# Optimization experiments

Hardware: AMD Instinct MI355X
Metric: run time of the kernel (lower is better)

Reference implementation:

```python
import jax, jax.numpy as jnp
import numpy as np

B, N, DIM = 4, 1024, 768
H, GP = 12, 64
HD = DIM // H
SCALE = HD ** -0.5


def setup_inputs() -> dict:
    key = jax.random.key(0)
    ks = jax.random.split(key, 7)
    s = DIM ** -0.5
    return {
        "x": jax.random.normal(ks[0], (B, N, DIM), dtype=jnp.float32),
        "W_qkv": jax.random.normal(ks[1], (3 * DIM, DIM), dtype=jnp.float32) * s,
        "b_qkv": jnp.zeros((3 * DIM,), dtype=jnp.float32),
        "W_gp": jax.random.normal(ks[2], (GP, DIM), dtype=jnp.float32) * s,
        "alpha": jax.random.normal(ks[3], (1, H, 1, 1), dtype=jnp.float32),
        "W_proj": jax.random.normal(ks[4], (DIM, DIM), dtype=jnp.float32) * s,
        "b_proj": jnp.zeros((DIM,), dtype=jnp.float32),
    }


def reference(x, W_qkv, b_qkv, W_gp, alpha, W_proj, b_proj):
    b, n, c = x.shape
    # qkv projection, split into heads: [b, h, n, hd]
    qkv = x @ W_qkv.T + b_qkv
    q, k, v = jnp.split(qkv, 3, axis=-1)
    def to_heads(t):
        return t.reshape(b, n, H, HD).transpose(0, 2, 1, 3)
    q, k, v = to_heads(q), to_heads(k), to_heads(v)

    # raw attention scores [b, h, n, n]
    attn = jnp.einsum('bhnd,bhmd->bhnm', q, k) * SCALE

    # group similarity: gp weight viewed as [h, gp, hd]
    gp = W_gp.reshape(H, GP, HD)
    gw = jnp.einsum('bhnd,hmd->bhnm', v, gp)          # [b, h, n, gp]
    gw = jax.nn.gelu(gw, approximate=False)           # exact GELU (torch default)
    gw = jax.nn.softmax(gw, axis=-1)
    G = jnp.einsum('bhnm,bhkm->bhnk', gw, gw)         # [b, h, n, n]

    # gated combination
    attn = jax.nn.softmax(attn * G, axis=-1)
    a = jax.nn.sigmoid(alpha)                          # [1, h, 1, 1]
    A = (1.0 - a) * attn + a * G
    # column-sum renormalization (sum over query dim 2)
    A = A / (A.sum(axis=2, keepdims=True) + 1e-8)

    out = jnp.einsum('bhnm,bhmd->bhnd', A, v)
    out = out.transpose(0, 2, 1, 3).reshape(b, n, c)
    return out @ W_proj.T + b_proj
```

## Files before the change

### kernel.cpp

```cpp
#include <hip/hip_runtime.h>
#include <math.h>

namespace {

constexpr int kN   = 1024;
constexpr int kDim = 768;
constexpr int kH   = 12;
constexpr int kBH  = 48;
constexpr float kScale = 0.125f;

typedef __attribute__((ext_vector_type(8))) short short8;
typedef __attribute__((ext_vector_type(4))) short short4v;
typedef __attribute__((ext_vector_type(4))) float f32x4;
typedef __attribute__((ext_vector_type(16))) float f32x16;
typedef __attribute__((ext_vector_type(4))) uint uint4v;

#define MFMA(a, b, c)   __builtin_amdgcn_mfma_f32_16x16x32_bf16(a, b, c, 0, 0, 0)
#define MFMA32(a, b, c) __builtin_amdgcn_mfma_f32_32x32x16_bf16(a, b, c, 0, 0, 0)

__device__ __forceinline__ ushort f2bf(float f) {
  uint u = __builtin_bit_cast(uint, f);
  u += 0x7fffu + ((u >> 16) & 1u);
  return (ushort)(u >> 16);
}
__device__ __forceinline__ float bf2f(ushort h) {
  uint u = ((uint)h) << 16;
  return __builtin_bit_cast(float, u);
}
__device__ __forceinline__ void split8(const float* f, short8& hi, short8& lo) {
  #pragma unroll
  for (int i = 0; i < 8; i++) {
    const ushort h = f2bf(f[i]);
    hi[i] = (short)h;
    lo[i] = (short)f2bf(f[i] - bf2f(h));
  }
}
__device__ __forceinline__ uint packbf(float a, float b) {
  return (uint)f2bf(a) | ((uint)f2bf(b) << 16);
}

__device__ __forceinline__ void gl16(const short* g, short* l) {
  __builtin_amdgcn_global_load_lds(
      (const __attribute__((address_space(1))) void*)g,
      (__attribute__((address_space(3))) void*)l, 16, 0, 0);
}

__device__ __forceinline__ short8 frag(const short* t, int row, int chunk) {
  return *(const short8*)(t + row * 64 + ((chunk ^ (row & 7)) << 3));
}

template<int ROWS, int W>
__device__ __forceinline__ void stage_tile(short* dst, const short* src,
                                           int stride, int w, int l) {
  #pragma unroll
  for (int c = 0; c < ROWS / 8; c += W) {
    const int cc = c + w;
    const int row0 = cc << 3;
    const int row = row0 + (l >> 3);
    const int ch = (l & 7) ^ (row & 7);
    gl16(src + (size_t)row * stride + (ch << 3), dst + row0 * 64);
  }
}

__global__ __launch_bounds__(256) void k_split(const float* __restrict__ src,
                                               short* __restrict__ h,
                                               short* __restrict__ l) {
  const size_t i = ((size_t)blockIdx.x * 256 + threadIdx.x) * 4;
  const float4 f = *(const float4*)(src + i);
  const float ff[4] = {f.x, f.y, f.z, f.w};
  short4v hv, lv;
  #pragma unroll
  for (int j = 0; j < 4; j++) {
    const ushort u = f2bf(ff[j]);
    hv[j] = (short)u;
    lv[j] = (short)f2bf(ff[j] - bf2f(u));
  }
  *(short4v*)(h + i) = hv;
  *(short4v*)(l + i) = lv;
}

__global__ __launch_bounds__(512) void k_qkv(const short* __restrict__ xh,
                                             const short* __restrict__ xl,
                                             const short* __restrict__ wh,
                                             const short* __restrict__ wl,
                                             const float* __restrict__ bias,
                                             short* __restrict__ qh, short* __restrict__ ql,
                                             short* __restrict__ kh, short* __restrict__ kl,
                                             short* __restrict__ vh, short* __restrict__ vl) {
  __shared__ __align__(16) short sb[2][32768];
  const int bx = blockIdx.x, by = blockIdx.y;
  const int tid = threadIdx.x, w = tid >> 6, lane = tid & 63;
  const int wr = w >> 2, wc = w & 3;
  const short* Asrc_h = xh + (size_t)(by * 128) * kDim;
  const short* Asrc_l = xl + (size_t)(by * 128) * kDim;
  const short* Bsrc_h = wh + (size_t)(bx * 128) * kDim;
  const short* Bsrc_l = wl + (size_t)(bx * 128) * kDim;

  f32x4 acc[4][2] = {};
  {
    short* nb = sb[0];
    stage_tile<128, 8>(nb,          Asrc_h, kDim, w, lane);
    stage_tile<128, 8>(nb + 8192,   Asrc_l, kDim, w, lane);
    stage_tile<128, 8>(nb + 16384,  Bsrc_h, kDim, w, lane);
    stage_tile<128, 8>(nb + 24576,  Bsrc_l, kDim, w, lane);
  }
  int p = 0;
  #pragma unroll 1
  for (int t = 0; t < 12; ++t) {
    __syncthreads();
    if (t < 11) {
      const int k0 = (t + 1) * 64;
      short* nb = sb[p ^ 1];
      stage_tile<128, 8>(nb,         Asrc_h + k0, kDim, w, lane);
      stage_tile<128, 8>(nb + 8192,  Asrc_l + k0, kDim, w, lane);
      stage_tile<128, 8>(nb + 16384, Bsrc_h + k0, kDim, w, lane);
      stage_tile<128, 8>(nb + 24576, Bsrc_l + k0, kDim, w, lane);
    }
    const short* cb = sb[p];
    #pragma unroll
    for (int s = 0; s < 2; ++s) {
      const int ch = (s << 2) + (lane >> 4);
      short8 af[4], alf[4], bf_[2], blf[2];
      #pragma unroll
      for (int i = 0; i < 4; i++) {
        const int ar = wr * 64 + i * 16 + (lane & 15);
        af[i]  = frag(cb, ar, ch);
        alf[i] = frag(cb + 8192, ar, ch);
      }
      #pragma unroll
      for (int j = 0; j < 2; j++) {
        const int br = wc * 32 + j * 16 + (lane & 15);
        bf_[j] = frag(cb + 16384, br, ch);
        blf[j] = frag(cb + 24576, br, ch);
      }
      #pragma unroll
      for (int i = 0; i < 4; i++)
        #pragma unroll
        for (int j = 0; j < 2; j++) {
          acc[i][j] = MFMA(af[i], bf_[j], acc[i][j]);
          acc[i][j] = MFMA(af[i], blf[j], acc[i][j]);
          acc[i][j] = MFMA(alf[i], bf_[j], acc[i][j]);
        }
    }
    p ^= 1;
  }
  #pragma unroll
  for (int j = 0; j < 2; j++) {
    const int col = bx * 128 + wc * 32 + j * 16 + (lane & 15);
    const int part = col / 768;
    const int rem = col - part * 768;
    const int hh = rem >> 6, d = rem & 63;
    short* dh = (part == 0) ? qh : ((part == 1) ? kh : vh);
    short* dl = (part == 0) ? ql : ((part == 1) ? kl : vl);
    const float bv = bias[col];
    const float scl = (part == 0) ? kScale : 1.0f;
    #pragma unroll
    for (int i = 0; i < 4; i++) {
      #pragma unroll
      for (int r = 0; r < 4; r++) {
        const int gr = by * 128 + wr * 64 + i * 16 + ((lane >> 4) << 2) + r;
        const int b = gr >> 10, n = gr & 1023;
        const float val = (acc[i][j][r] + bv) * scl;
        const ushort hu = f2bf(val);
        const size_t idx = (size_t)((b * kH + hh) * kN + n) * 64 + d;
        dh[idx] = (short)hu;
        dl[idx] = (short)f2bf(val - bf2f(hu));
      }
    }
  }
}

__global__ __launch_bounds__(512) void k_gw(const short* __restrict__ vh,
                                            const short* __restrict__ vl,
                                            const float* __restrict__ Wgp,
                                            short* __restrict__ gwh,
                                            short* __restrict__ gwl) {
  const int bh = blockIdx.x;
  const int h = bh % kH;
  const int n0 = blockIdx.y << 7;
  const int tid = threadIdx.x, w = tid >> 6, lane = tid & 63;
  __shared__ __align__(16) short gph[4096], gpl[4096];
  {
    const int r = tid >> 3, c = tid & 7;
    float f[8] __attribute__((aligned(16)));
    *(float4*)(f + 0) = *(const float4*)(Wgp + h * 4096 + r * 64 + c * 8);
    *(float4*)(f + 4) = *(const float4*)(Wgp + h * 4096 + r * 64 + c * 8 + 4);
    short8 hh, ll;
    split8(f, hh, ll);
    const int slot = c ^ (r & 7);
    *(short8*)(gph + r * 64 + slot * 8) = hh;
    *(short8*)(gpl + r * 64 + slot * 8) = ll;
  }
  short8 vhf[2], vlf[2];
  const size_t arow = (size_t)(bh * kN + n0 + w * 16 + (lane & 15)) * 64 + ((lane >> 4) << 3);
  vhf[0] = *(const short8*)(vh + arow); vhf[1] = *(const short8*)(vh + arow + 32);
  vlf[0] = *(const short8*)(vl + arow); vlf[1] = *(const short8*)(vl + arow + 32);
  __syncthreads();

  f32x4 aU[4] = {};
  #pragma unroll
  for (int msub = 0; msub < 4; msub++) {
    #pragma unroll
    for (int s = 0; s < 2; s++) {
      const int row = (msub << 4) + (lane & 15);
      const int ch = (s << 2) + (lane >> 4);
      const short8 bh_ = frag(gph, row, ch);
      const short8 bl_ = frag(gpl, row, ch);
      aU[msub] = MFMA(vhf[s], bh_, aU[msub]);
      aU[msub] = MFMA(vhf[s], bl_, aU[msub]);
      aU[msub] = MFMA(vlf[s], bh_, aU[msub]);
    }
  }
  #pragma unroll
  for (int r = 0; r < 4; r++) {
    float u[4];
    #pragma unroll
    for (int m = 0; m < 4; m++) {
      const float a = aU[m][r];
      u[m] = 0.5f * a * (1.0f + erff(a * 0.70710678118654752f));
    }
    float mx = fmaxf(fmaxf(u[0], u[1]), fmaxf(u[2], u[3]));
    #pragma unroll
    for (int msk = 1; msk < 16; msk <<= 1) mx = fmaxf(mx, __shfl_xor(mx, msk));
    float e[4], ssum = 0.f;
    #pragma unroll
    for (int m = 0; m < 4; m++) { e[m] = __expf(u[m] - mx); ssum += e[m]; }
    #pragma unroll
    for (int msk = 1; msk < 16; msk <<= 1) ssum += __shfl_xor(ssum, msk);
    const float inv = 1.0f / ssum;
    const int n = n0 + w * 16 + ((lane >> 4) << 2) + r;
    #pragma unroll
    for (int m = 0; m < 4; m++) {
      const float g = e[m] * inv;
      const ushort hu = f2bf(g);
      const size_t idx = (size_t)(bh * kN + n) * 64 + (m << 4) + (lane & 15);
      gwh[idx] = (short)hu;
      gwl[idx] = (short)f2bf(g - bf2f(hu));
    }
  }
}

__global__ __launch_bounds__(256) void k_vt(const short* __restrict__ vh,
                                            const float* __restrict__ rcolv,
                                            short* __restrict__ vtg) {
  const int bh = blockIdx.x;
  const int n0 = blockIdx.y << 6;
  __shared__ short t[64][80];
  const int tid = threadIdx.x;
  {
    const int n = tid >> 2, d0 = (tid & 3) << 4;
    const float rc = rcolv[bh * kN + n0 + n];
    const short8 a = *(const short8*)(vh + (size_t)(bh * kN + n0 + n) * 64 + d0);
    const short8 b = *(const short8*)(vh + (size_t)(bh * kN + n0 + n) * 64 + d0 + 8);
    #pragma unroll
    for (int i = 0; i < 8; ++i) {
      t[d0 + i][n]     = (short)f2bf(bf2f((ushort)a[i]) * rc);
      t[d0 + 8 + i][n] = (short)f2bf(bf2f((ushort)b[i]) * rc);
    }
  }
  __syncthreads();
  const int d = tid >> 2, j0 = (tid & 3) << 4;
  short* dst = vtg + (size_t)bh * 65536 + (size_t)d * 1024 + n0 + j0;
  *(short8*)(dst)     = *(const short8*)(&t[d][j0]);
  *(short8*)(dst + 8) = *(const short8*)(&t[d][j0 + 8]);
}

__global__ __launch_bounds__(256, 3) void k_denom(const short* __restrict__ qh,
                                                  const short* __restrict__ ql,
                                                  const short* __restrict__ kh,
                                                  const short* __restrict__ kl,
                                                  const short* __restrict__ gwh,
                                                  const short* __restrict__ gwl,
                                                  float* __restrict__ rdenom) {
  const int bh = blockIdx.x;
  const int n0 = blockIdx.y << 6;
  const int tid = threadIdx.x, w = tid >> 6, lane = tid & 63;
  const int lc = lane & 31, hl = lane >> 5;
  const int nw = w & 1, mh = w >> 1;
  __shared__ __align__(16) short sb[32768];
  __shared__ float part[4][32];
  const short* my = sb + mh * 16384;

  short8 qB[4], qlB[4], gB[4], glB[4];
  {
    const size_t nrow = (size_t)(bh * kN + n0 + nw * 32 + lc) * 64;
    #pragma unroll
    for (int ks = 0; ks < 4; ks++) {
      const int off = ks * 16 + (hl << 3);
      qB[ks]  = *(const short8*)(qh  + nrow + off);
      qlB[ks] = *(const short8*)(ql  + nrow + off);
      gB[ks]  = *(const short8*)(gwh + nrow + off);
      glB[ks] = *(const short8*)(gwl + nrow + off);
    }
  }
  float dsum = 0.f;
  #pragma unroll 1
  for (int t = 0; t < 8; ++t) {
    __syncthreads();
    const size_t mo0 = (size_t)(bh * kN + t * 64) * 64;
    const size_t mo1 = (size_t)(bh * kN + 512 + t * 64) * 64;
    stage_tile<64, 4>(sb,          kh  + mo0, 64, w, lane);
    stage_tile<64, 4>(sb + 4096,   kl  + mo0, 64, w, lane);
    stage_tile<64, 4>(sb + 8192,   gwh + mo0, 64, w, lane);
    stage_tile<64, 4>(sb + 12288,  gwl + mo0, 64, w, lane);
    stage_tile<64, 4>(sb + 16384,  kh  + mo1, 64, w, lane);
    stage_tile<64, 4>(sb + 20480,  kl  + mo1, 64, w, lane);
    stage_tile<64, 4>(sb + 24576,  gwh + mo1, 64, w, lane);
    stage_tile<64, 4>(sb + 28672,  gwl + mo1, 64, w, lane);
    __syncthreads();
    #pragma unroll
    for (int at = 0; at < 2; ++at) {
      f32x16 aS = {}, aG = {};
      #pragma unroll
      for (int ks = 0; ks < 4; ++ks) {
        const int row = at * 32 + lc;
        const int ck = ks * 2 + hl;
        const short8 Ah_ = frag(my, row, ck);
        const short8 Al_ = frag(my + 4096, row, ck);
        const short8 Eh_ = frag(my + 8192, row, ck);
        const short8 El_ = frag(my + 12288, row, ck);
        aS = MFMA32(Ah_, qB[ks], aS);
        aS = MFMA32(Al_, qB[ks], aS);
        aS = MFMA32(Ah_, qlB[ks], aS);
        aG = MFMA32(Eh_, gB[ks], aG);
        aG = MFMA32(El_, gB[ks], aG);
        aG = MFMA32(Eh_, glB[ks], aG);
      }
      #pragma unroll
      for (int r = 0; r < 16; ++r)
        dsum += __expf(aS[r] * aG[r]);
    }
  }
  dsum += __shfl_xor(dsum, 32);
  if (hl == 0) part[w][lc] = dsum;
  __syncthreads();
  if (tid < 64)
    rdenom[bh * kN + n0 + tid] =
        1.0f / (part[tid >> 5][tid & 31] + part[2 + (tid >> 5)][tid & 31]);
}

__global__ __launch_bounds__(256, 3) void k_colsum(const short* __restrict__ qh,
                                                   const short* __restrict__ ql,
                                                   const short* __restrict__ kh,
                                                   const short* __restrict__ kl,
                                                   const short* __restrict__ gwh,
                                                   const short* __restrict__ gwl,
                                                   const float* __restrict__ rdenom,
                                                   const float* __restrict__ alpha,
                                                   float* __restrict__ rcolv) {
  const int bh = blockIdx.x;
  const int m0 = blockIdx.y << 6;
  const int tid = threadIdx.x, w = tid >> 6, lane = tid & 63;
  const int lc = lane & 31, hl = lane >> 5;
  const int mw = w & 1, nh = w >> 1;
  __shared__ __align__(16) short sb[32768];
  __shared__ float part[4][32];
  __shared__ float rdl[2][64];
  const short* my = sb + nh * 16384;
  const float ah_ = 1.0f / (1.0f + __expf(-alpha[bh % kH]));
  const float om = 1.0f - ah_;

  short8 kB[4], klB[4], gB[4], glB[4];
  {
    const size_t mrow = (size_t)(bh * kN + m0 + mw * 32 + lc) * 64;
    #pragma unroll
    for (int ks = 0; ks < 4; ks++) {
      const int off = ks * 16 + (hl << 3);
      kB[ks]  = *(const short8*)(kh  + mrow + off);
      klB[ks] = *(const short8*)(kl  + mrow + off);
      gB[ks]  = *(const short8*)(gwh + mrow + off);
      glB[ks] = *(const short8*)(gwl + mrow + off);
    }
  }
  float csum = 0.f;
  #pragma unroll 1
  for (int t = 0; t < 8; ++t) {
    __syncthreads();
    const size_t no0 = (size_t)(bh * kN + t * 64) * 64;
    const size_t no1 = (size_t)(bh * kN + 512 + t * 64) * 64;
    stage_tile<64, 4>(sb,          qh  + no0, 64, w, lane);
    stage_tile<64, 4>(sb + 4096,   ql  + no0, 64, w, lane);
    stage_tile<64, 4>(sb + 8192,   gwh + no0, 64, w, lane);
    stage_tile<64, 4>(sb + 12288,  gwl + no0, 64, w, lane);
    stage_tile<64, 4>(sb + 16384,  qh  + no1, 64, w, lane);
    stage_tile<64, 4>(sb + 20480,  ql  + no1, 64, w, lane);
    stage_tile<64, 4>(sb + 24576,  gwh + no1, 64, w, lane);
    stage_tile<64, 4>(sb + 28672,  gwl + no1, 64, w, lane);
    if (tid < 128)
      rdl[tid >> 6][tid & 63] =
          rdenom[bh * kN + (tid >> 6) * 512 + t * 64 + (tid & 63)];
    __syncthreads();
    #pragma unroll
    for (int at = 0; at < 2; ++at) {
      f32x16 aS = {}, aG = {};
      #pragma unroll
      for (int ks = 0; ks < 4; ++ks) {
        const int row = at * 32 + lc;
        const int ck = ks * 2 + hl;
        const short8 Ah_ = frag(my, row, ck);
        const short8 Al_ = frag(my + 4096, row, ck);
        const short8 Eh_ = frag(my + 8192, row, ck);
        const short8 El_ = frag(my + 12288, row, ck);
        aS = MFMA32(Ah_, kB[ks], aS);
        aS = MFMA32(Al_, kB[ks], aS);
        aS = MFMA32(Ah_, klB[ks], aS);
        aG = MFMA32(Eh_, gB[ks], aG);
        aG = MFMA32(El_, gB[ks], aG);
        aG = MFMA32(Eh_, glB[ks], aG);
      }
      #pragma unroll
      for (int r = 0; r < 16; ++r) {
        const int nr = at * 32 + (r & 3) + ((r >> 2) << 3) + (hl << 2);
        const float g = aG[r];
        csum += om * (__expf(aS[r] * g) * rdl[nh][nr]) + ah_ * g;
      }
    }
  }
  csum += __shfl_xor(csum, 32);
  if (hl == 0) part[w][lc] = csum;
  __syncthreads();
  if (tid < 64)
    rcolv[bh * kN + m0 + tid] =
        1.0f / (part[tid >> 5][tid & 31] + part[2 + (tid >> 5)][tid & 31] + 1e-8f);
}

__global__ __launch_bounds__(512, 2) void k_out(const short* __restrict__ qh,
                                                const short* __restrict__ ql,
                                                const short* __restrict__ kh,
                                                const short* __restrict__ kl,
                                                const short* __restrict__ vtg,
                                                const short* __restrict__ gwh,
                                                const short* __restrict__ gwl,
                                                const float* __restrict__ rdenom,
                                                const float* __restrict__ alpha,
                                                short* __restrict__ ctxh,
                                                short* __restrict__ ctxl) {
  const int bh = blockIdx.x;
  const int h = bh % kH;
  const int b = bh / kH;
  const int n0 = blockIdx.y << 7;
  const int tid = threadIdx.x, w = tid >> 6, lane = tid & 63;
  const int lc = lane & 31, hl = lane >> 5;
  const int nw = w & 3, mh = w >> 2;
  __shared__ __align__(16) short sb[40960];
  const float ah_ = 1.0f / (1.0f + __expf(-alpha[h]));
  const float om = 1.0f - ah_;
  const short* my = sb + mh * 20480;

  short8 qB[4], qlB[4], gB[4], glB[4];
  {
    const size_t nrow = (size_t)(bh * kN + n0 + nw * 32 + lc) * 64;
    #pragma unroll
    for (int ks = 0; ks < 4; ks++) {
      const int off = ks * 16 + (hl << 3);
      qB[ks]  = *(const short8*)(qh  + nrow + off);
      qlB[ks] = *(const short8*)(ql  + nrow + off);
      gB[ks]  = *(const short8*)(gwh + nrow + off);
      glB[ks] = *(const short8*)(gwl + nrow + off);
    }
  }
  const float rdn = rdenom[bh * kN + n0 + nw * 32 + lc];
  f32x16 oac[2] = {};

  #pragma unroll 1
  for (int t = 0; t < 8; ++t) {
    __syncthreads();
    const size_t mo0 = (size_t)(bh * kN + t * 64) * 64;
    const size_t mo1 = (size_t)(bh * kN + 512 + t * 64) * 64;
    stage_tile<64, 8>(sb,          kh  + mo0, 64, w, lane);
    stage_tile<64, 8>(sb + 4096,   kl  + mo0, 64, w, lane);
    stage_tile<64, 8>(sb + 8192,   gwh + mo0, 64, w, lane);
    stage_tile<64, 8>(sb + 12288,  gwl + mo0, 64, w, lane);
    stage_tile<64, 8>(sb + 16384,  vtg + (size_t)bh * 65536 + t * 64, kN, w, lane);
    stage_tile<64, 8>(sb + 20480,  kh  + mo1, 64, w, lane);
    stage_tile<64, 8>(sb + 24576,  kl  + mo1, 64, w, lane);
    stage_tile<64, 8>(sb + 28672,  gwh + mo1, 64, w, lane);
    stage_tile<64, 8>(sb + 32768,  gwl + mo1, 64, w, lane);
    stage_tile<64, 8>(sb + 36864,  vtg + (size_t)bh * 65536 + 512 + t * 64, kN, w, lane);
    __syncthreads();
    short8 pf[4];
    #pragma unroll
    for (int at = 0; at < 2; ++at) {
      f32x16 aS = {}, aG = {};
      #pragma unroll
      for (int ks = 0; ks < 4; ++ks) {
        const int row = at * 32 + lc;
        const int ck = ks * 2 + hl;
        const short8 Ah_ = frag(my, row, ck);
        const short8 Al_ = frag(my + 4096, row, ck);
        const short8 Eh_ = frag(my + 8192, row, ck);
        const short8 El_ = frag(my + 12288, row, ck);
        aS = MFMA32(Ah_, qB[ks], aS);
        aS = MFMA32(Al_, qB[ks], aS);
        aS = MFMA32(Ah_, qlB[ks], aS);
        aG = MFMA32(Eh_, gB[ks], aG);
        aG = MFMA32(El_, gB[ks], aG);
        aG = MFMA32(Eh_, glB[ks], aG);
      }
      float a[16];
      #pragma unroll
      for (int r = 0; r < 16; ++r) {
        const float g = aG[r];
        const float p = __expf(aS[r] * g) * rdn;
        a[r] = om * p + ah_ * g;
      }
      uint W[8], Ws[8];
      #pragma unroll
      for (int j = 0; j < 8; ++j) W[j] = packbf(a[2 * j], a[2 * j + 1]);
      #pragma unroll
      for (int j = 0; j < 8; ++j) Ws[j] = __shfl_xor(W[j], 32);
      {
        uint4v b0, b1;
        b0[0] = hl ? Ws[2] : W[0];  b0[1] = hl ? Ws[3] : W[1];
        b0[2] = hl ? W[2]  : Ws[0]; b0[3] = hl ? W[3]  : Ws[1];
        b1[0] = hl ? Ws[6] : W[4];  b1[1] = hl ? Ws[7] : W[5];
        b1[2] = hl ? W[6]  : Ws[4]; b1[3] = hl ? W[7]  : Ws[5];
        pf[at * 2 + 0] = __builtin_bit_cast(short8, b0);
        pf[at * 2 + 1] = __builtin_bit_cast(short8, b1);
      }
    }
    #pragma unroll
    for (int dt = 0; dt < 2; ++dt)
      #pragma unroll
      for (int ks = 0; ks < 4; ++ks) {
        const short8 va = frag(my + 16384, dt * 32 + lc, ks * 2 + hl);
        oac[dt] = MFMA32(va, pf[ks], oac[dt]);
      }
  }
  __syncthreads();
  float* buf = (float*)sb;
  if (mh == 1) {
    #pragma unroll
    for (int dt = 0; dt < 2; ++dt)
      #pragma unroll
      for (int r = 0; r < 16; ++r) {
        const int d = dt * 32 + (r & 3) + ((r >> 2) << 3) + (hl << 2);
        buf[(nw * 32 + lc) * 68 + d] = oac[dt][r];
      }
  }
  __syncthreads();
  if (mh == 0) {
    #pragma unroll
    for (int dt = 0; dt < 2; ++dt)
      #pragma unroll
      for (int r = 0; r < 16; ++r) {
        const int d = dt * 32 + (r & 3) + ((r >> 2) << 3) + (hl << 2);
        const int idx = (nw * 32 + lc) * 68 + d;
        buf[idx] = oac[dt][r] + buf[idx];
      }
  }
  __syncthreads();
  {
    const int rowi = tid >> 2;
    const int d0 = (tid & 3) << 4;
    float f[16] __attribute__((aligned(16)));
    #pragma unroll
    for (int j = 0; j < 4; ++j)
      *(float4*)(f + 4 * j) = *(const float4*)(&buf[rowi * 68 + d0 + 4 * j]);
    const int n = n0 + rowi;
    short* dsth = ctxh + (size_t)(b * kN + n) * kDim + h * 64 + d0;
    short* dstl = ctxl + (size_t)(b * kN + n) * kDim + h * 64 + d0;
    #pragma unroll
    for (int g8 = 0; g8 < 2; ++g8) {
      short8 hi, lo;
      split8(f + 8 * g8, hi, lo);
      *(short8*)(dsth + 8 * g8) = hi;
      *(short8*)(dstl + 8 * g8) = lo;
    }
  }
}

__global__ __launch_bounds__(512) void k_proj(const short* __restrict__ ch_,
                                              const short* __restrict__ cl_,
                                              const short* __restrict__ wh,
                                              const short* __restrict__ wl,
                                              const float* __restrict__ bias,
                                              float* __restrict__ out) {
  __shared__ __align__(16) short sb[2][32768];
  const int bx = blockIdx.x, by = blockIdx.y;
  const int tid = threadIdx.x, w = tid >> 6, lane = tid & 63;
  const int wr = w >> 2, wc = w & 3;
  const short* Asrc_h = ch_ + (size_t)(by * 128) * kDim;
  const short* Asrc_l = cl_ + (size_t)(by * 128) * kDim;
  const short* Bsrc_h = wh + (size_t)(bx * 128) * kDim;
  const short* Bsrc_l = wl + (size_t)(bx * 128) * kDim;

  f32x4 acc[4][2] = {};
  {
    short* nb = sb[0];
    stage_tile<128, 8>(nb,         Asrc_h, kDim, w, lane);
    stage_tile<128, 8>(nb + 8192,  Asrc_l, kDim, w, lane);
    stage_tile<128, 8>(nb + 16384, Bsrc_h, kDim, w, lane);
    stage_tile<128, 8>(nb + 24576, Bsrc_l, kDim, w, lane);
  }
  int p = 0;
  #pragma unroll 1
  for (int t = 0; t < 12; ++t) {
    __syncthreads();
    if (t < 11) {
      const int k0 = (t + 1) * 64;
      short* nb = sb[p ^ 1];
      stage_tile<128, 8>(nb,         Asrc_h + k0, kDim, w, lane);
      stage_tile<128, 8>(nb + 8192,  Asrc_l + k0, kDim, w, lane);
      stage_tile<128, 8>(nb + 16384, Bsrc_h + k0, kDim, w, lane);
      stage_tile<128, 8>(nb + 24576, Bsrc_l + k0, kDim, w, lane);
    }
    const short* cb = sb[p];
    #pragma unroll
    for (int s = 0; s < 2; ++s) {
      const int ch = (s << 2) + (lane >> 4);
      short8 af[4], alf[4], bf_[2], blf[2];
      #pragma unroll
      for (int i = 0; i < 4; i++) {
        const int ar = wr * 64 + i * 16 + (lane & 15);
        af[i]  = frag(cb, ar, ch);
        alf[i] = frag(cb + 8192, ar, ch);
      }
      #pragma unroll
      for (int j = 0; j < 2; j++) {
        const int br = wc * 32 + j * 16 + (lane & 15);
        bf_[j] = frag(cb + 16384, br, ch);
        blf[j] = frag(cb + 24576, br, ch);
      }
      #pragma unroll
      for (int i = 0; i < 4; i++)
        #pragma unroll
        for (int j = 0; j < 2; j++) {
          acc[i][j] = MFMA(af[i], bf_[j], acc[i][j]);
          acc[i][j] = MFMA(af[i], blf[j], acc[i][j]);
          acc[i][j] = MFMA(alf[i], bf_[j], acc[i][j]);
          acc[i][j] = MFMA(alf[i], blf[j], acc[i][j]);
        }
    }
    p ^= 1;
  }
  #pragma unroll
  for (int j = 0; j < 2; j++) {
    const int col = bx * 128 + wc * 32 + j * 16 + (lane & 15);
    const float bv = bias[col];
    #pragma unroll
    for (int i = 0; i < 4; i++) {
      #pragma unroll
      for (int r = 0; r < 4; r++) {
        const int row = by * 128 + wr * 64 + i * 16 + ((lane >> 4) << 2) + r;
        out[(size_t)row * kDim + col] = acc[i][j][r] + bv;
      }
    }
  }
}

}

extern "C" void kernel_launch(void* const* d_in, const int* in_sizes, int n_in,
                              void* d_out, int out_size, void* d_ws, size_t ws_size,
                              hipStream_t stream) {
  const float* x     = (const float*)d_in[0];
  const float* Wqkv  = (const float*)d_in[1];
  const float* bqkv  = (const float*)d_in[2];
  const float* Wgp   = (const float*)d_in[3];
  const float* alpha = (const float*)d_in[4];
  const float* Wproj = (const float*)d_in[5];
  const float* bproj = (const float*)d_in[6];
  float* out = (float*)d_out;

  const size_t he = 3145728;
  short* qh  = (short*)d_ws;
  short* ql  = qh + he;
  short* kh  = ql + he;
  short* kl  = kh + he;
  short* vh  = kl + he;
  short* vl  = vh + he;
  short* gwh = vl + he;
  short* gwl = gwh + he;
  short* xh  = gwl + he;
  short* xl  = xh + he;
  float* rdenom = (float*)(xl + he);
  float* rcolv  = rdenom + (size_t)kBH * kN;

  short* Wqh = gwh;  short* Wql = gwl;
  short* vtg = vl;
  short* ctxh = xh;  short* ctxl = xl;
  short* Wph = qh;   short* Wpl = ql;

  k_split<<<3072, 256, 0, stream>>>(x, xh, xl);
  k_split<<<1728, 256, 0, stream>>>(Wqkv, Wqh, Wql);
  k_qkv  <<<dim3(18, 32), 512, 0, stream>>>(xh, xl, Wqh, Wql, bqkv,
                                            qh, ql, kh, kl, vh, vl);
  k_gw   <<<dim3(kBH, 8), 512, 0, stream>>>(vh, vl, Wgp, gwh, gwl);
  k_denom<<<dim3(kBH, 16), 256, 0, stream>>>(qh, ql, kh, kl, gwh, gwl, rdenom);
  k_colsum<<<dim3(kBH, 16), 256, 0, stream>>>(qh, ql, kh, kl, gwh, gwl,
                                              rdenom, alpha, rcolv);
  k_vt   <<<dim3(kBH, 16), 256, 0, stream>>>(vh, rcolv, vtg);
  k_out  <<<dim3(kBH, 8), 512, 0, stream>>>(qh, ql, kh, kl, vtg, gwh, gwl,
                                            rdenom, alpha, ctxh, ctxl);
  k_split<<<576, 256, 0, stream>>>(Wproj, Wph, Wpl);
  k_proj <<<dim3(6, 32), 512, 0, stream>>>(ctxh, ctxl, Wph, Wpl, bproj, out);
}
```

Before: 277.8 us.

## Halve key-tile size in attention kernels to shrink LDS and raise occupancy

The denom, colsum and output kernels now stage 32-row key tiles, one per half of the split key range, over 16 iterations instead of 64-row tiles over 8. This halves shared memory per block so more blocks fit per CU. k_out also drops from 512-thread, 128-query blocks to 256-thread, 64-query blocks with twice as many blocks, and loads the V^T tile with a swizzled direct global-to-LDS copy. The cost is twice as many barriers and staging rounds per block, and K/gw tiles are now reloaded by twice as many k_out blocks.

```diff
diff --git a/kernel.cpp b/kernel.cpp
--- a/kernel.cpp
+++ b/kernel.cpp
@@ -277,9 +277,8 @@
   const int tid = threadIdx.x, w = tid >> 6, lane = tid & 63;
   const int lc = lane & 31, hl = lane >> 5;
   const int nw = w & 1, mh = w >> 1;
-  __shared__ __align__(16) short sb[32768];
+  __shared__ __align__(16) short sb[16384];
   __shared__ float part[4][32];
-  const short* my = sb + mh * 16384;
 
   short8 qB[4], qlB[4], gB[4], glB[4];
   {
@@ -295,41 +294,38 @@
   }
   float dsum = 0.f;
   #pragma unroll 1
-  for (int t = 0; t < 8; ++t) {
-    __syncthreads();
-    const size_t mo0 = (size_t)(bh * kN + t * 64) * 64;
-    const size_t mo1 = (size_t)(bh * kN + 512 + t * 64) * 64;
-    stage_tile<64, 4>(sb,          kh  + mo0, 64, w, lane);
-    stage_tile<64, 4>(sb + 4096,   kl  + mo0, 64, w, lane);
-    stage_tile<64, 4>(sb + 8192,   gwh + mo0, 64, w, lane);
-    stage_tile<64, 4>(sb + 12288,  gwl + mo0, 64, w, lane);
-    stage_tile<64, 4>(sb + 16384,  kh  + mo1, 64, w, lane);
-    stage_tile<64, 4>(sb + 20480,  kl  + mo1, 64, w, lane);
-    stage_tile<64, 4>(sb + 24576,  gwh + mo1, 64, w, lane);
-    stage_tile<64, 4>(sb + 28672,  gwl + mo1, 64, w, lane);
-    __syncthreads();
-    #pragma unroll
-    for (int at = 0; at < 2; ++at) {
-      f32x16 aS = {}, aG = {};
-      #pragma unroll
-      for (int ks = 0; ks < 4; ++ks) {
-        const int row = at * 32 + lc;
-        const int ck = ks * 2 + hl;
-        const short8 Ah_ = frag(my, row, ck);
-        const short8 Al_ = frag(my + 4096, row, ck);
-        const short8 Eh_ = frag(my + 8192, row, ck);
-        const short8 El_ = frag(my + 12288, row, ck);
-        aS = MFMA32(Ah_, qB[ks], aS);
-        aS = MFMA32(Al_, qB[ks], aS);
-        aS = MFMA32(Ah_, qlB[ks], aS);
-        aG = MFMA32(Eh_, gB[ks], aG);
-        aG = MFMA32(El_, gB[ks], aG);
-        aG = MFMA32(Eh_, glB[ks], aG);
-      }
-      #pragma unroll
-      for (int r = 0; r < 16; ++r)
-        dsum += __expf(aS[r] * aG[r]);
-    }
+  for (int t = 0; t < 16; ++t) {
+    __syncthreads();
+    const size_t mo0 = (size_t)(bh * kN + t * 32) * 64;
+    const size_t mo1 = (size_t)(bh * kN + 512 + t * 32) * 64;
+    stage_tile<32, 4>(sb,                kh  + mo0, 64, w, lane);
+    stage_tile<32, 4>(sb + 2048,         kh  + mo1, 64, w, lane);
+    stage_tile<32, 4>(sb + 4096,         kl  + mo0, 64, w, lane);
+    stage_tile<32, 4>(sb + 4096 + 2048,  kl  + mo1, 64, w, lane);
+    stage_tile<32, 4>(sb + 8192,         gwh + mo0, 64, w, lane);
+    stage_tile<32, 4>(sb + 8192 + 2048,  gwh + mo1, 64, w, lane);
+    stage_tile<32, 4>(sb + 12288,        gwl + mo0, 64, w, lane);
+    stage_tile<32, 4>(sb + 12288 + 2048, gwl + mo1, 64, w, lane);
+    __syncthreads();
+    f32x16 aS = {}, aG = {};
+    #pragma unroll
+    for (int ks = 0; ks < 4; ++ks) {
+      const int row = mh * 32 + lc;
+      const int ck = ks * 2 + hl;
+      const short8 Ah_ = frag(sb, row, ck);
+      const short8 Al_ = frag(sb + 4096, row, ck);
+      const short8 Eh_ = frag(sb + 8192, row, ck);
+      const short8 El_ = frag(sb + 12288, row, ck);
+      aS = MFMA32(Ah_, qB[ks], aS);
+      aS = MFMA32(Al_, qB[ks], aS);
+      aS = MFMA32(Ah_, qlB[ks], aS);
+      aG = MFMA32(Eh_, gB[ks], aG);
+      aG = MFMA32(El_, gB[ks], aG);
+      aG = MFMA32(Eh_, glB[ks], aG);
+    }
+    #pragma unroll
+    for (int r = 0; r < 16; ++r)
+      dsum += __expf(aS[r] * aG[r]);
   }
   dsum += __shfl_xor(dsum, 32);
   if (hl == 0) part[w][lc] = dsum;
@@ -353,10 +349,9 @@
   const int tid = threadIdx.x, w = tid >> 6, lane = tid & 63;
   const int lc = lane & 31, hl = lane >> 5;
   const int mw = w & 1, nh = w >> 1;
-  __shared__ __align__(16) short sb[32768];
+  __shared__ __align__(16) short sb[16384];
   __shared__ float part[4][32];
-  __shared__ float rdl[2][64];
-  const short* my = sb + nh * 16384;
+  __shared__ float rdl[2][32];
   const float ah_ = 1.0f / (1.0f + __expf(-alpha[bh % kH]));
   const float om = 1.0f - ah_;
 
@@ -374,46 +369,43 @@
   }
   float csum = 0.f;
   #pragma unroll 1
-  for (int t = 0; t < 8; ++t) {
-    __syncthreads();
-    const size_t no0 = (size_t)(bh * kN + t * 64) * 64;
-    const size_t no1 = (size_t)(bh * kN + 512 + t * 64) * 64;
-    stage_tile<64, 4>(sb,          qh  + no0, 64, w, lane);
-    stage_tile<64, 4>(sb + 4096,   ql  + no0, 64, w, lane);
-    stage_tile<64, 4>(sb + 8192,   gwh + no0, 64, w, lane);
-    stage_tile<64, 4>(sb + 12288,  gwl + no0, 64, w, lane);
-    stage_tile<64, 4>(sb + 16384,  qh  + no1, 64, w, lane);
-    stage_tile<64, 4>(sb + 20480,  ql  + no1, 64, w, lane);
-    stage_tile<64, 4>(sb + 24576,  gwh + no1, 64, w, lane);
-    stage_tile<64, 4>(sb + 28672,  gwl + no1, 64, w, lane);
-    if (tid < 128)
-      rdl[tid >> 6][tid & 63] =
-          rdenom[bh * kN + (tid >> 6) * 512 + t * 64 + (tid & 63)];
-    __syncthreads();
-    #pragma unroll
-    for (int at = 0; at < 2; ++at) {
-      f32x16 aS = {}, aG = {};
-      #pragma unroll
-      for (int ks = 0; ks < 4; ++ks) {
-        const int row = at * 32 + lc;
-        const int ck = ks * 2 + hl;
-        const short8 Ah_ = frag(my, row, ck);
-        const short8 Al_ = frag(my + 4096, row, ck);
-        const short8 Eh_ = frag(my + 8192, row, ck);
-        const short8 El_ = frag(my + 12288, row, ck);
-        aS = MFMA32(Ah_, kB[ks], aS);
-        aS = MFMA32(Al_, kB[ks], aS);
-        aS = MFMA32(Ah_, klB[ks], aS);
-        aG = MFMA32(Eh_, gB[ks], aG);
-        aG = MFMA32(El_, gB[ks], aG);
-        aG = MFMA32(Eh_, glB[ks], aG);
-      }
-      #pragma unroll
-      for (int r = 0; r < 16; ++r) {
-        const int nr = at * 32 + (r & 3) + ((r >> 2) << 3) + (hl << 2);
-        const float g = aG[r];
-        csum += om * (__expf(aS[r] * g) * rdl[nh][nr]) + ah_ * g;
-      }
+  for (int t = 0; t < 16; ++t) {
+    __syncthreads();
+    const size_t no0 = (size_t)(bh * kN + t * 32) * 64;
+    const size_t no1 = (size_t)(bh * kN + 512 + t * 32) * 64;
+    stage_tile<32, 4>(sb,                qh  + no0, 64, w, lane);
+    stage_tile<32, 4>(sb + 2048,         qh  + no1, 64, w, lane);
+    stage_tile<32, 4>(sb + 4096,         ql  + no0, 64, w, lane);
+    stage_tile<32, 4>(sb + 4096 + 2048,  ql  + no1, 64, w, lane);
+    stage_tile<32, 4>(sb + 8192,         gwh + no0, 64, w, lane);
+    stage_tile<32, 4>(sb + 8192 + 2048,  gwh + no1, 64, w, lane);
+    stage_tile<32, 4>(sb + 12288,        gwl + no0, 64, w, lane);
+    stage_tile<32, 4>(sb + 12288 + 2048, gwl + no1, 64, w, lane);
+    if (tid < 64)
+      rdl[tid >> 5][tid & 31] =
+          rdenom[bh * kN + (tid >> 5) * 512 + t * 32 + (tid & 31)];
+    __syncthreads();
+    f32x16 aS = {}, aG = {};
+    #pragma unroll
+    for (int ks = 0; ks < 4; ++ks) {
+      const int row = nh * 32 + lc;
+      const int ck = ks * 2 + hl;
+      const short8 Ah_ = frag(sb, row, ck);
+      const short8 Al_ = frag(sb + 4096, row, ck);
+      const short8 Eh_ = frag(sb + 8192, row, ck);
+      const short8 El_ = frag(sb + 12288, row, ck);
+      aS = MFMA32(Ah_, kB[ks], aS);
+      aS = MFMA32(Al_, kB[ks], aS);
+      aS = MFMA32(Ah_, klB[ks], aS);
+      aG = MFMA32(Eh_, gB[ks], aG);
+      aG = MFMA32(El_, gB[ks], aG);
+      aG = MFMA32(Eh_, glB[ks], aG);
+    }
+    #pragma unroll
+    for (int r = 0; r < 16; ++r) {
+      const int nr = (r & 3) + ((r >> 2) << 3) + (hl << 2);
+      const float g = aG[r];
+      csum += om * (__expf(aS[r] * g) * rdl[nh][nr]) + ah_ * g;
     }
   }
   csum += __shfl_xor(csum, 32);
@@ -424,7 +416,7 @@
         1.0f / (part[tid >> 5][tid & 31] + part[2 + (tid >> 5)][tid & 31] + 1e-8f);
 }
 
-__global__ __launch_bounds__(512, 2) void k_out(const short* __restrict__ qh,
+__global__ __launch_bounds__(256, 3) void k_out(const short* __restrict__ qh,
                                                 const short* __restrict__ ql,
                                                 const short* __restrict__ kh,
                                                 const short* __restrict__ kl,
@@ -438,14 +430,13 @@
   const int bh = blockIdx.x;
   const int h = bh % kH;
   const int b = bh / kH;
-  const int n0 = blockIdx.y << 7;
+  const int n0 = blockIdx.y << 6;
   const int tid = threadIdx.x, w = tid >> 6, lane = tid & 63;
   const int lc = lane & 31, hl = lane >> 5;
-  const int nw = w & 3, mh = w >> 2;
-  __shared__ __align__(16) short sb[40960];
+  const int nw = w & 1, mh = w >> 1;
+  __shared__ __align__(16) short sb[20480];
   const float ah_ = 1.0f / (1.0f + __expf(-alpha[h]));
   const float om = 1.0f - ah_;
-  const short* my = sb + mh * 20480;
 
   short8 qB[4], qlB[4], gB[4], glB[4];
   {
@@ -460,70 +451,75 @@
     }
   }
   const float rdn = rdenom[bh * kN + n0 + nw * 32 + lc];
+  const short* vbh = vtg + (size_t)bh * 65536;
   f32x16 oac[2] = {};
 
   #pragma unroll 1
-  for (int t = 0; t < 8; ++t) {
-    __syncthreads();
-    const size_t mo0 = (size_t)(bh * kN + t * 64) * 64;
-    const size_t mo1 = (size_t)(bh * kN + 512 + t * 64) * 64;
-    stage_tile<64, 8>(sb,          kh  + mo0, 64, w, lane);
-    stage_tile<64, 8>(sb + 4096,   kl  + mo0, 64, w, lane);
-    stage_tile<64, 8>(sb + 8192,   gwh + mo0, 64, w, lane);
-    stage_tile<64, 8>(sb + 12288,  gwl + mo0, 64, w, lane);
-    stage_tile<64, 8>(sb + 16384,  vtg + (size_t)bh * 65536 + t * 64, kN, w, lane);
-    stage_tile<64, 8>(sb + 20480,  kh  + mo1, 64, w, lane);
-    stage_tile<64, 8>(sb + 24576,  kl  + mo1, 64, w, lane);
-    stage_tile<64, 8>(sb + 28672,  gwh + mo1, 64, w, lane);
-    stage_tile<64, 8>(sb + 32768,  gwl + mo1, 64, w, lane);
-    stage_tile<64, 8>(sb + 36864,  vtg + (size_t)bh * 65536 + 512 + t * 64, kN, w, lane);
-    __syncthreads();
-    short8 pf[4];
-    #pragma unroll
-    for (int at = 0; at < 2; ++at) {
-      f32x16 aS = {}, aG = {};
-      #pragma unroll
-      for (int ks = 0; ks < 4; ++ks) {
-        const int row = at * 32 + lc;
-        const int ck = ks * 2 + hl;
-        const short8 Ah_ = frag(my, row, ck);
-        const short8 Al_ = frag(my + 4096, row, ck);
-        const short8 Eh_ = frag(my + 8192, row, ck);
-        const short8 El_ = frag(my + 12288, row, ck);
-        aS = MFMA32(Ah_, qB[ks], aS);
-        aS = MFMA32(Al_, qB[ks], aS);
-        aS = MFMA32(Ah_, qlB[ks], aS);
-        aG = MFMA32(Eh_, gB[ks], aG);
-        aG = MFMA32(El_, gB[ks], aG);
-        aG = MFMA32(Eh_, glB[ks], aG);
-      }
-      float a[16];
-      #pragma unroll
-      for (int r = 0; r < 16; ++r) {
-        const float g = aG[r];
-        const float p = __expf(aS[r] * g) * rdn;
-        a[r] = om * p + ah_ * g;
-      }
+  for (int t = 0; t < 16; ++t) {
+    __syncthreads();
+    const size_t mo0 = (size_t)(bh * kN + t * 32) * 64;
+    const size_t mo1 = (size_t)(bh * kN + 512 + t * 32) * 64;
+    stage_tile<32, 4>(sb,                kh  + mo0, 64, w, lane);
+    stage_tile<32, 4>(sb + 2048,         kh  + mo1, 64, w, lane);
+    stage_tile<32, 4>(sb + 4096,         kl  + mo0, 64, w, lane);
+    stage_tile<32, 4>(sb + 4096 + 2048,  kl  + mo1, 64, w, lane);
+    stage_tile<32, 4>(sb + 8192,         gwh + mo0, 64, w, lane);
+    stage_tile<32, 4>(sb + 8192 + 2048,  gwh + mo1, 64, w, lane);
+    stage_tile<32, 4>(sb + 12288,        gwl + mo0, 64, w, lane);
+    stage_tile<32, 4>(sb + 12288 + 2048, gwl + mo1, 64, w, lane);
+    #pragma unroll
+    for (int c = 0; c < 8; c += 4) {
+      const int cc = c + w;
+      const int row0 = cc << 3;
+      const int row = row0 + (lane >> 3);
+      const int ch = (lane & 7) ^ (row & 7);
+      const int mg = ((ch >> 2) ? 512 : 0) + t * 32 + ((ch & 3) << 3);
+      gl16(vbh + (size_t)row * 1024 + mg, sb + 16384 + row0 * 64);
+    }
+    __syncthreads();
+    f32x16 aS = {}, aG = {};
+    #pragma unroll
+    for (int ks = 0; ks < 4; ++ks) {
+      const int row = mh * 32 + lc;
+      const int ck = ks * 2 + hl;
+      const short8 Ah_ = frag(sb, row, ck);
+      const short8 Al_ = frag(sb + 4096, row, ck);
+      const short8 Eh_ = frag(sb + 8192, row, ck);
+      const short8 El_ = frag(sb + 12288, row, ck);
+      aS = MFMA32(Ah_, qB[ks], aS);
+      aS = MFMA32(Al_, qB[ks], aS);
+      aS = MFMA32(Ah_, qlB[ks], aS);
+      aG = MFMA32(Eh_, gB[ks], aG);
+      aG = MFMA32(El_, gB[ks], aG);
+      aG = MFMA32(Eh_, glB[ks], aG);
+    }
+    float a[16];
+    #pragma unroll
+    for (int r = 0; r < 16; ++r) {
+      const float g = aG[r];
+      const float p = __expf(aS[r] * g) * rdn;
+      a[r] = om * p + ah_ * g;
+    }
+    short8 pf[2];
+    {
       uint W[8], Ws[8];
       #pragma unroll
       for (int j = 0; j < 8; ++j) W[j] = packbf(a[2 * j], a[2 * j + 1]);
       #pragma unroll
       for (int j = 0; j < 8; ++j) Ws[j] = __shfl_xor(W[j], 32);
-      {
-        uint4v b0, b1;
-        b0[0] = hl ? Ws[2] : W[0];  b0[1] = hl ? Ws[3] : W[1];
-        b0[2] = hl ? W[2]  : Ws[0]; b0[3] = hl ? W[3]  : Ws[1];
-        b1[0] = hl ? Ws[6] : W[4];  b1[1] = hl ? Ws[7] : W[5];
-        b1[2] = hl ? W[6]  : Ws[4]; b1[3] = hl ? W[7]  : Ws[5];
-        pf[at * 2 + 0] = __builtin_bit_cast(short8, b0);
-        pf[at * 2 + 1] = __builtin_bit_cast(short8, b1);
-      }
+      uint4v b0, b1;
+      b0[0] = hl ? Ws[2] : W[0];  b0[1] = hl ? Ws[3] : W[1];
+      b0[2] = hl ? W[2]  : Ws[0]; b0[3] = hl ? W[3]  : Ws[1];
+      b1[0] = hl ? Ws[6] : W[4];  b1[1] = hl ? Ws[7] : W[5];
+      b1[2] = hl ? W[6]  : Ws[4]; b1[3] = hl ? W[7]  : Ws[5];
+      pf[0] = __builtin_bit_cast(short8, b0);
+      pf[1] = __builtin_bit_cast(short8, b1);
     }
     #pragma unroll
     for (int dt = 0; dt < 2; ++dt)
       #pragma unroll
-      for (int ks = 0; ks < 4; ++ks) {
-        const short8 va = frag(my + 16384, dt * 32 + lc, ks * 2 + hl);
+      for (int ks = 0; ks < 2; ++ks) {
+        const short8 va = frag(sb + 16384, dt * 32 + lc, mh * 4 + ks * 2 + hl);
         oac[dt] = MFMA32(va, pf[ks], oac[dt]);
       }
   }
@@ -691,8 +687,8 @@
   k_colsum<<<dim3(kBH, 16), 256, 0, stream>>>(qh, ql, kh, kl, gwh, gwl,
                                               rdenom, alpha, rcolv);
   k_vt   <<<dim3(kBH, 16), 256, 0, stream>>>(vh, rcolv, vtg);
-  k_out  <<<dim3(kBH, 8), 512, 0, stream>>>(qh, ql, kh, kl, vtg, gwh, gwl,
-                                            rdenom, alpha, ctxh, ctxl);
+  k_out  <<<dim3(kBH, 16), 256, 0, stream>>>(qh, ql, kh, kl, vtg, gwh, gwl,
+                                             rdenom, alpha, ctxh, ctxl);
   k_split<<<576, 256, 0, stream>>>(Wproj, Wph, Wpl);
   k_proj <<<dim3(6, 32), 512, 0, stream>>>(ctxh, ctxl, Wph, Wpl, bproj, out);
 }
```

After: 253.7 us. -8.7%, faster.
